# Performance work log

Measured on AMD Instinct MI355X. Metric: run time of the kernel, lower is better.

Reference implementation:

```python
import jax, jax.numpy as jnp
import numpy as np

N_NODES = 50000
N_EDGES = 600000
IN_DIM, HID, OUT_DIM = 128, 128, 64
LN_EPS = 1e-5


def setup_inputs() -> dict:
    key = jax.random.key(0)
    ks = jax.random.split(key, 10)
    def glorot(k, shape):
        lim = np.sqrt(6.0 / (shape[0] + shape[1]))
        return jax.random.uniform(k, shape, jnp.float32, -lim, lim)
    return {
        "x": jax.random.normal(ks[0], (N_NODES, IN_DIM), jnp.float32),
        "src": jax.random.randint(ks[1], (N_EDGES,), 0, N_NODES, jnp.int32),
        "dst": jax.random.randint(ks[2], (N_EDGES,), 0, N_NODES, jnp.int32),
        "W0": glorot(ks[3], (IN_DIM, HID)), "b0": jnp.zeros((HID,), jnp.float32),
        "W1": glorot(ks[4], (HID, HID)),    "b1": jnp.zeros((HID,), jnp.float32),
        "W2": glorot(ks[5], (HID, OUT_DIM)),"b2": jnp.zeros((OUT_DIM,), jnp.float32),
        "ln_scale": jnp.ones((HID,), jnp.float32),
        "ln_bias": jnp.zeros((HID,), jnp.float32),
    }


def _degree_norms(src, dst):
    ones = jnp.ones((src.shape[0],), jnp.float32)
    deg_out = jax.ops.segment_sum(ones, src, num_segments=N_NODES)
    deg_in = jax.ops.segment_sum(ones, dst, num_segments=N_NODES)
    # DGL clamps degree to min 1 for norm='both'
    out_norm = jnp.clip(deg_out, 1.0, None) ** -0.5
    in_norm = jnp.clip(deg_in, 1.0, None) ** -0.5
    return out_norm, in_norm


def _graph_conv(h, src, dst, out_norm, in_norm, W, b):
    # norm='both': scale src side, SpMM aggregate, scale dst side, then affine
    h = h * out_norm[:, None]
    h = h @ W  # apply weight first (mathematically identical, smaller messages when out<in)
    agg = jax.ops.segment_sum(h[src], dst, num_segments=N_NODES)  # [N, D]
    return agg * in_norm[:, None] + b


def _layernorm(h, scale, bias):
    mu = jnp.mean(h, axis=-1, keepdims=True)
    var = jnp.var(h, axis=-1, keepdims=True)
    return (h - mu) * jax.lax.rsqrt(var + LN_EPS) * scale + bias


def reference(x, src, dst, W0, b0, W1, b1, W2, b2, ln_scale, ln_bias):
    out_norm, in_norm = _degree_norms(src, dst)
    # dropout is identity in eval mode
    h = jax.nn.relu(_graph_conv(x, src, dst, out_norm, in_norm, W0, b0))
    h = _layernorm(h, ln_scale, ln_bias)
    h = jax.nn.relu(_graph_conv(h, src, dst, out_norm, in_norm, W1, b1))
    h = _layernorm(h, ln_scale, ln_bias)
    # last layer: encoding=True -> keep activation; no norm after last layer
    h = jax.nn.relu(_graph_conv(h, src, dst, out_norm, in_norm, W2, b2))
    return h
```

## Files before the change

kernel.cpp:

```cpp
#include <hip/hip_runtime.h>
#include <hip/hip_fp16.h>

#define NN 50000
#define NE 600000
#define LN_EPS 1e-5f
#define SCAN_B 49
#define RANGES 8
#define RSZ 6250
#define CHUNKS 16
#define CSZ 37500

typedef __attribute__((ext_vector_type(8))) _Float16 half8;
typedef __attribute__((ext_vector_type(4))) float floatx4;

__device__ __align__(16) __half g_h0[NN * 128];
__device__ __align__(16) __half g_h1[NN * 128];
__device__ __align__(16) int g_deg_in[NN];
__device__ float g_out_norm[NN];
__device__ float g_in_norm[NN];
__device__ int g_rowptr[NN + 1];
__device__ int g_esrc[NE];
__device__ int g_blocksum[SCAN_B];
__device__ int g_blockoff[SCAN_B];
__device__ int g_pout[CHUNKS * NN];
__device__ int g_pin[CHUNKS * NN];
__device__ int g_base[CHUNKS * NN];

__device__ __forceinline__ __half* hbuf(int i) { return i ? g_h1 : g_h0; }

__global__ __launch_bounds__(256) void histo_kernel(const int* __restrict__ src,
                                                    const int* __restrict__ dst) {
    __shared__ int h_out[RSZ];
    __shared__ int h_in[RSZ];
    int c = blockIdx.x / RANGES, r = blockIdx.x % RANGES;
    int lo = r * RSZ;
    for (int i = threadIdx.x; i < RSZ; i += 256) { h_out[i] = 0; h_in[i] = 0; }
    __syncthreads();
    const int4* s4 = (const int4*)(src + c * CSZ);
    const int4* d4 = (const int4*)(dst + c * CSZ);
    for (int i = threadIdx.x; i < CSZ / 4; i += 256) {
        int4 s = s4[i], d = d4[i];
        int v;
        v = s.x - lo; if ((unsigned)v < RSZ) atomicAdd(&h_out[v], 1);
        v = s.y - lo; if ((unsigned)v < RSZ) atomicAdd(&h_out[v], 1);
        v = s.z - lo; if ((unsigned)v < RSZ) atomicAdd(&h_out[v], 1);
        v = s.w - lo; if ((unsigned)v < RSZ) atomicAdd(&h_out[v], 1);
        v = d.x - lo; if ((unsigned)v < RSZ) atomicAdd(&h_in[v], 1);
        v = d.y - lo; if ((unsigned)v < RSZ) atomicAdd(&h_in[v], 1);
        v = d.z - lo; if ((unsigned)v < RSZ) atomicAdd(&h_in[v], 1);
        v = d.w - lo; if ((unsigned)v < RSZ) atomicAdd(&h_in[v], 1);
    }
    __syncthreads();
    for (int i = threadIdx.x; i < RSZ; i += 256) {
        g_pout[c * NN + lo + i] = h_out[i];
        g_pin[c * NN + lo + i]  = h_in[i];
    }
}

__global__ __launch_bounds__(256) void sums_norms_kernel() {
    int n = blockIdx.x * 256 + threadIdx.x;
    if (n >= NN) return;
    int so = 0, si = 0;
#pragma unroll
    for (int c = 0; c < CHUNKS; ++c) { so += g_pout[c * NN + n]; si += g_pin[c * NN + n]; }
    g_deg_in[n] = si;
    g_out_norm[n] = rsqrtf((float)max(so, 1));
    g_in_norm[n]  = rsqrtf((float)max(si, 1));
}

__global__ __launch_bounds__(256) void scan_phase1() {
    __shared__ int wsum[4];
    int b = blockIdx.x, t = threadIdx.x;
    int base = b * 1024 + t * 4;
    int s = 0;
    if (base + 3 < NN) {
        int4 v = *(const int4*)&g_deg_in[base];
        s = v.x + v.y + v.z + v.w;
    } else {
#pragma unroll
        for (int k = 0; k < 4; ++k)
            if (base + k < NN) s += g_deg_in[base + k];
    }
#pragma unroll
    for (int off = 32; off; off >>= 1) s += __shfl_xor(s, off, 64);
    if ((t & 63) == 0) wsum[t >> 6] = s;
    __syncthreads();
    if (t == 0) g_blocksum[b] = wsum[0] + wsum[1] + wsum[2] + wsum[3];
}

__global__ __launch_bounds__(64) void scan_phase2() {
    int lane = threadIdx.x;
    int own = (lane < SCAN_B) ? g_blocksum[lane] : 0;
    int v = own;
#pragma unroll
    for (int off = 1; off < 64; off <<= 1) {
        int n = __shfl_up(v, off, 64);
        if (lane >= off) v += n;
    }
    if (lane < SCAN_B) g_blockoff[lane] = v - own;
    if (lane == SCAN_B - 1) g_rowptr[NN] = v;
}

__global__ __launch_bounds__(256) void scan_phase3() {
    __shared__ int sums[256];
    int b = blockIdx.x, t = threadIdx.x;
    int base = b * 1024 + t * 4;
    int v[4];
#pragma unroll
    for (int k = 0; k < 4; ++k) v[k] = (base + k < NN) ? g_deg_in[base + k] : 0;
    int tsum = v[0] + v[1] + v[2] + v[3];
    sums[t] = tsum;
    __syncthreads();
    for (int off = 1; off < 256; off <<= 1) {
        int add = (t >= off) ? sums[t - off] : 0;
        __syncthreads();
        sums[t] += add;
        __syncthreads();
    }
    int excl = sums[t] - tsum + g_blockoff[b];
#pragma unroll
    for (int k = 0; k < 4; ++k) {
        int idx = base + k;
        if (idx < NN) g_rowptr[idx] = excl;
        excl += v[k];
    }
}

__global__ __launch_bounds__(256) void base_kernel() {
    int n = blockIdx.x * 256 + threadIdx.x;
    if (n >= NN) return;
    int run = g_rowptr[n];
#pragma unroll
    for (int c = 0; c < CHUNKS; ++c) {
        g_base[c * NN + n] = run;
        run += g_pin[c * NN + n];
    }
}

__global__ __launch_bounds__(256) void place_lds_kernel(const int* __restrict__ src,
                                                        const int* __restrict__ dst) {
    __shared__ int cur[RSZ];
    int c = blockIdx.x / RANGES, r = blockIdx.x % RANGES;
    int lo = r * RSZ;
    for (int i = threadIdx.x; i < RSZ; i += 256) cur[i] = g_base[c * NN + lo + i];
    __syncthreads();
    const int4* s4 = (const int4*)(src + c * CSZ);
    const int4* d4 = (const int4*)(dst + c * CSZ);
    for (int i = threadIdx.x; i < CSZ / 4; i += 256) {
        int4 s = s4[i], d = d4[i];
        int v, p;
        v = d.x - lo; if ((unsigned)v < RSZ) { p = atomicAdd(&cur[v], 1); g_esrc[p] = s.x; }
        v = d.y - lo; if ((unsigned)v < RSZ) { p = atomicAdd(&cur[v], 1); g_esrc[p] = s.y; }
        v = d.z - lo; if ((unsigned)v < RSZ) { p = atomicAdd(&cur[v], 1); g_esrc[p] = s.z; }
        v = d.w - lo; if ((unsigned)v < RSZ) { p = atomicAdd(&cur[v], 1); g_esrc[p] = s.w; }
    }
}

template <int N, bool AEXT>
__global__ __launch_bounds__(256) void gemm_mfma(const float* __restrict__ Aext,
                                                 int a_ib, int c_ib,
                                                 const float* __restrict__ Wg,
                                                 int M) {
    constexpr int NT = N / 16;
    constexpr int LOGN = (N == 128) ? 7 : 6;
    __shared__ _Float16 Wl[128 * N];

    const int tid = threadIdx.x;
    for (int e = tid; e < 128 * N; e += 256) {
        int k = e >> LOGN, n = e & (N - 1);
        Wl[(((k >> 3) * N + n) << 3) + (k & 7)] = (_Float16)Wg[e];
    }
    __syncthreads();

    const int wv = tid >> 6, lane = tid & 63;
    const int quad = lane >> 4, mrow = lane & 15;
    const int rowbase = blockIdx.x * 64 + wv * 16;
    const int arow0 = rowbase + mrow;
    const int arow = (arow0 < M) ? arow0 : (M - 1);

    floatx4 acc[NT] = {};
    const __half* Ah = AEXT ? nullptr : hbuf(a_ib);

#pragma unroll
    for (int kk = 0; kk < 4; ++kk) {
        const int k0 = kk * 32 + quad * 8;
        half8 afrag;
        if (AEXT) {
            const float4* ap = (const float4*)(Aext + (size_t)arow * 128 + k0);
            float4 f0 = ap[0], f1 = ap[1];
            afrag[0] = (_Float16)f0.x; afrag[1] = (_Float16)f0.y;
            afrag[2] = (_Float16)f0.z; afrag[3] = (_Float16)f0.w;
            afrag[4] = (_Float16)f1.x; afrag[5] = (_Float16)f1.y;
            afrag[6] = (_Float16)f1.z; afrag[7] = (_Float16)f1.w;
        } else {
            afrag = *(const half8*)(Ah + (size_t)arow * 128 + k0);
        }
#pragma unroll
        for (int nt = 0; nt < NT; ++nt) {
            half8 bfrag = *(const half8*)&Wl[(((kk * 4 + quad) * N + nt * 16 + mrow) << 3)];
            acc[nt] = __builtin_amdgcn_mfma_f32_16x16x32_f16(afrag, bfrag, acc[nt], 0, 0, 0);
        }
    }

    __half* C = hbuf(c_ib);
#pragma unroll
    for (int r = 0; r < 4; ++r) {
        int crow = rowbase + quad * 4 + r;
        if (crow < M) {
            float s = g_out_norm[crow];
#pragma unroll
            for (int nt = 0; nt < NT; ++nt) {
                float v = acc[nt][r] * s;
                C[(size_t)crow * N + nt * 16 + mrow] = __float2half_rn(v);
            }
        }
    }
}

__global__ __launch_bounds__(256) void gather_ln_kernel(int s_ib, int d_ib,
                                                        const float* __restrict__ b,
                                                        const float* __restrict__ ln_s,
                                                        const float* __restrict__ ln_b) {
    int wave = threadIdx.x >> 6;
    int lane = threadIdx.x & 63;
    int node = blockIdx.x * 4 + wave;
    if (node >= NN) return;
    const unsigned int* Hu = (const unsigned int*)hbuf(s_ib);
    int beg = g_rowptr[node], end = g_rowptr[node + 1];
    float ax = 0.f, ay = 0.f;
    int j = beg;
    for (; j + 3 < end; j += 4) {
        int s0 = g_esrc[j], s1 = g_esrc[j + 1], s2 = g_esrc[j + 2], s3 = g_esrc[j + 3];
        unsigned int u0 = Hu[s0 * 64 + lane];
        unsigned int u1 = Hu[s1 * 64 + lane];
        unsigned int u2 = Hu[s2 * 64 + lane];
        unsigned int u3 = Hu[s3 * 64 + lane];
        float2 f0 = __half22float2(*(const __half2*)&u0);
        float2 f1 = __half22float2(*(const __half2*)&u1);
        float2 f2 = __half22float2(*(const __half2*)&u2);
        float2 f3 = __half22float2(*(const __half2*)&u3);
        ax += (f0.x + f1.x) + (f2.x + f3.x);
        ay += (f0.y + f1.y) + (f2.y + f3.y);
    }
    for (; j < end; ++j) {
        unsigned int u = Hu[g_esrc[j] * 64 + lane];
        float2 f = __half22float2(*(const __half2*)&u);
        ax += f.x; ay += f.y;
    }
    float nrm = g_in_norm[node];
    int c = lane * 2;
    float vx = fmaxf(ax * nrm + b[c], 0.f);
    float vy = fmaxf(ay * nrm + b[c + 1], 0.f);
    float s = vx + vy;
    float sq = vx * vx + vy * vy;
#pragma unroll
    for (int off = 32; off > 0; off >>= 1) {
        s  += __shfl_xor(s, off, 64);
        sq += __shfl_xor(sq, off, 64);
    }
    float mean = s * (1.f / 128.f);
    float var = sq * (1.f / 128.f) - mean * mean;
    float inv = rsqrtf(var + LN_EPS);
    float ox = (vx - mean) * inv * ln_s[c] + ln_b[c];
    float oy = (vy - mean) * inv * ln_s[c + 1] + ln_b[c + 1];
    __half2 h = __floats2half2_rn(ox, oy);
    ((unsigned int*)hbuf(d_ib))[node * 64 + lane] = *(const unsigned int*)&h;
}

__global__ __launch_bounds__(256) void GCN_63831803953156_kernel(int s_ib,
                                                                 const float* __restrict__ b2,
                                                                 float* __restrict__ out) {
    int wave = threadIdx.x >> 6;
    int lane = threadIdx.x & 63;
    int node = blockIdx.x * 4 + wave;
    if (node >= NN) return;
    const unsigned short* Hs = (const unsigned short*)hbuf(s_ib);
    int beg = g_rowptr[node], end = g_rowptr[node + 1];
    float acc = 0.f;
    int j = beg;
    for (; j + 3 < end; j += 4) {
        int s0 = g_esrc[j], s1 = g_esrc[j + 1], s2 = g_esrc[j + 2], s3 = g_esrc[j + 3];
        unsigned short u0 = Hs[s0 * 64 + lane];
        unsigned short u1 = Hs[s1 * 64 + lane];
        unsigned short u2 = Hs[s2 * 64 + lane];
        unsigned short u3 = Hs[s3 * 64 + lane];
        acc += (__half2float(*(const __half*)&u0) + __half2float(*(const __half*)&u1)) +
               (__half2float(*(const __half*)&u2) + __half2float(*(const __half*)&u3));
    }
    for (; j < end; ++j) {
        unsigned short u = Hs[g_esrc[j] * 64 + lane];
        acc += __half2float(*(const __half*)&u);
    }
    float v = fmaxf(acc * g_in_norm[node] + b2[lane], 0.f);
    out[node * 64 + lane] = v;
}

extern "C" void kernel_launch(void* const* d_in, const int* in_sizes, int n_in,
                              void* d_out, int out_size, void* d_ws, size_t ws_size,
                              hipStream_t stream) {
    const float* x   = (const float*)d_in[0];
    const int* src   = (const int*)d_in[1];
    const int* dst   = (const int*)d_in[2];
    const float* W0  = (const float*)d_in[3];
    const float* b0  = (const float*)d_in[4];
    const float* W1  = (const float*)d_in[5];
    const float* b1  = (const float*)d_in[6];
    const float* W2  = (const float*)d_in[7];
    const float* b2  = (const float*)d_in[8];
    const float* ln_s = (const float*)d_in[9];
    const float* ln_b = (const float*)d_in[10];
    (void)d_ws; (void)ws_size; (void)in_sizes; (void)n_in; (void)out_size;

    histo_kernel<<<CHUNKS * RANGES, 256, 0, stream>>>(src, dst);
    sums_norms_kernel<<<(NN + 255) / 256, 256, 0, stream>>>();
    scan_phase1<<<SCAN_B, 256, 0, stream>>>();
    scan_phase2<<<1, 64, 0, stream>>>();
    scan_phase3<<<SCAN_B, 256, 0, stream>>>();
    base_kernel<<<(NN + 255) / 256, 256, 0, stream>>>();
    place_lds_kernel<<<CHUNKS * RANGES, 256, 0, stream>>>(src, dst);

    const int GB = (NN + 63) / 64;

    gemm_mfma<128, true><<<GB, 256, 0, stream>>>(x, -1, 0, W0, NN);
    gather_ln_kernel<<<(NN + 3) / 4, 256, 0, stream>>>(0, 1, b0, ln_s, ln_b);

    gemm_mfma<128, false><<<GB, 256, 0, stream>>>(nullptr, 1, 0, W1, NN);
    gather_ln_kernel<<<(NN + 3) / 4, 256, 0, stream>>>(0, 1, b1, ln_s, ln_b);

    gemm_mfma<64, false><<<GB, 256, 0, stream>>>(nullptr, 1, 0, W2, NN);
    GCN_63831803953156_kernel<<<(NN + 3) / 4, 256, 0, stream>>>(0, b2, (float*)d_out);
}
```

Baseline: 286.0 us.

## Gather multiple nodes per wave with wider loads and fuse CSR-build kernels

The gather kernels now split each 64-lane wave into sub-groups that each process a separate node, reading 8-byte vectors per lane instead of 2- or 4-byte values. This doubles or quadruples the number of independent rows in flight per wave and widens the memory transactions. The degree-sum, norm and scan-phase1 kernels are merged into one 1024-thread kernel, and the base-offset computation is folded into scan phase 3, which removes two launches. The node bounds checks are dropped, so correctness relies on NN being divisible by 8 and 16.

```diff
diff --git a/kernel.cpp b/kernel.cpp
--- a/kernel.cpp
+++ b/kernel.cpp
@@ -57,35 +57,30 @@
     }
 }
 
-__global__ __launch_bounds__(256) void sums_norms_kernel() {
-    int n = blockIdx.x * 256 + threadIdx.x;
-    if (n >= NN) return;
-    int so = 0, si = 0;
-#pragma unroll
-    for (int c = 0; c < CHUNKS; ++c) { so += g_pout[c * NN + n]; si += g_pin[c * NN + n]; }
-    g_deg_in[n] = si;
-    g_out_norm[n] = rsqrtf((float)max(so, 1));
-    g_in_norm[n]  = rsqrtf((float)max(si, 1));
-}
-
-__global__ __launch_bounds__(256) void scan_phase1() {
-    __shared__ int wsum[4];
+__global__ __launch_bounds__(1024) void deg_scan1_kernel() {
+    __shared__ int wsum[16];
     int b = blockIdx.x, t = threadIdx.x;
-    int base = b * 1024 + t * 4;
-    int s = 0;
-    if (base + 3 < NN) {
-        int4 v = *(const int4*)&g_deg_in[base];
-        s = v.x + v.y + v.z + v.w;
-    } else {
-#pragma unroll
-        for (int k = 0; k < 4; ++k)
-            if (base + k < NN) s += g_deg_in[base + k];
-    }
+    int n = b * 1024 + t;
+    int si = 0;
+    if (n < NN) {
+        int so = 0;
+#pragma unroll
+        for (int c = 0; c < CHUNKS; ++c) { so += g_pout[c * NN + n]; si += g_pin[c * NN + n]; }
+        g_deg_in[n] = si;
+        g_out_norm[n] = rsqrtf((float)max(so, 1));
+        g_in_norm[n]  = rsqrtf((float)max(si, 1));
+    }
+    int s = si;
 #pragma unroll
     for (int off = 32; off; off >>= 1) s += __shfl_xor(s, off, 64);
     if ((t & 63) == 0) wsum[t >> 6] = s;
     __syncthreads();
-    if (t == 0) g_blocksum[b] = wsum[0] + wsum[1] + wsum[2] + wsum[3];
+    if (t < 16) {
+        int v = wsum[t];
+#pragma unroll
+        for (int off = 8; off; off >>= 1) v += __shfl_xor(v, off, 16);
+        if (t == 0) g_blocksum[b] = v;
+    }
 }
 
 __global__ __launch_bounds__(64) void scan_phase2() {
@@ -101,7 +96,7 @@
     if (lane == SCAN_B - 1) g_rowptr[NN] = v;
 }
 
-__global__ __launch_bounds__(256) void scan_phase3() {
+__global__ __launch_bounds__(256) void scan3_base_kernel() {
     __shared__ int sums[256];
     int b = blockIdx.x, t = threadIdx.x;
     int base = b * 1024 + t * 4;
@@ -121,19 +116,16 @@
 #pragma unroll
     for (int k = 0; k < 4; ++k) {
         int idx = base + k;
-        if (idx < NN) g_rowptr[idx] = excl;
+        if (idx < NN) {
+            g_rowptr[idx] = excl;
+            int run = excl;
+#pragma unroll
+            for (int c = 0; c < CHUNKS; ++c) {
+                g_base[c * NN + idx] = run;
+                run += g_pin[c * NN + idx];
+            }
+        }
         excl += v[k];
-    }
-}
-
-__global__ __launch_bounds__(256) void base_kernel() {
-    int n = blockIdx.x * 256 + threadIdx.x;
-    if (n >= NN) return;
-    int run = g_rowptr[n];
-#pragma unroll
-    for (int c = 0; c < CHUNKS; ++c) {
-        g_base[c * NN + n] = run;
-        run += g_pin[c * NN + n];
     }
 }
 
@@ -223,48 +215,58 @@
                                                         const float* __restrict__ ln_b) {
     int wave = threadIdx.x >> 6;
     int lane = threadIdx.x & 63;
-    int node = blockIdx.x * 4 + wave;
-    if (node >= NN) return;
-    const unsigned int* Hu = (const unsigned int*)hbuf(s_ib);
+    int sub = lane >> 5, sl = lane & 31;
+    int node = blockIdx.x * 8 + wave * 2 + sub;
+    const uint2* Hu = (const uint2*)hbuf(s_ib);
     int beg = g_rowptr[node], end = g_rowptr[node + 1];
-    float ax = 0.f, ay = 0.f;
+    float a0 = 0.f, a1 = 0.f, a2 = 0.f, a3 = 0.f;
     int j = beg;
     for (; j + 3 < end; j += 4) {
         int s0 = g_esrc[j], s1 = g_esrc[j + 1], s2 = g_esrc[j + 2], s3 = g_esrc[j + 3];
-        unsigned int u0 = Hu[s0 * 64 + lane];
-        unsigned int u1 = Hu[s1 * 64 + lane];
-        unsigned int u2 = Hu[s2 * 64 + lane];
-        unsigned int u3 = Hu[s3 * 64 + lane];
-        float2 f0 = __half22float2(*(const __half2*)&u0);
-        float2 f1 = __half22float2(*(const __half2*)&u1);
-        float2 f2 = __half22float2(*(const __half2*)&u2);
-        float2 f3 = __half22float2(*(const __half2*)&u3);
-        ax += (f0.x + f1.x) + (f2.x + f3.x);
-        ay += (f0.y + f1.y) + (f2.y + f3.y);
+        uint2 u0 = Hu[s0 * 32 + sl];
+        uint2 u1 = Hu[s1 * 32 + sl];
+        uint2 u2 = Hu[s2 * 32 + sl];
+        uint2 u3 = Hu[s3 * 32 + sl];
+        float2 p0 = __half22float2(*(const __half2*)&u0.x), q0 = __half22float2(*(const __half2*)&u0.y);
+        float2 p1 = __half22float2(*(const __half2*)&u1.x), q1 = __half22float2(*(const __half2*)&u1.y);
+        float2 p2 = __half22float2(*(const __half2*)&u2.x), q2 = __half22float2(*(const __half2*)&u2.y);
+        float2 p3 = __half22float2(*(const __half2*)&u3.x), q3 = __half22float2(*(const __half2*)&u3.y);
+        a0 += (p0.x + p1.x) + (p2.x + p3.x);
+        a1 += (p0.y + p1.y) + (p2.y + p3.y);
+        a2 += (q0.x + q1.x) + (q2.x + q3.x);
+        a3 += (q0.y + q1.y) + (q2.y + q3.y);
     }
     for (; j < end; ++j) {
-        unsigned int u = Hu[g_esrc[j] * 64 + lane];
-        float2 f = __half22float2(*(const __half2*)&u);
-        ax += f.x; ay += f.y;
+        uint2 u = Hu[g_esrc[j] * 32 + sl];
+        float2 p = __half22float2(*(const __half2*)&u.x), q = __half22float2(*(const __half2*)&u.y);
+        a0 += p.x; a1 += p.y; a2 += q.x; a3 += q.y;
     }
     float nrm = g_in_norm[node];
-    int c = lane * 2;
-    float vx = fmaxf(ax * nrm + b[c], 0.f);
-    float vy = fmaxf(ay * nrm + b[c + 1], 0.f);
-    float s = vx + vy;
-    float sq = vx * vx + vy * vy;
-#pragma unroll
-    for (int off = 32; off > 0; off >>= 1) {
+    float4 bb = ((const float4*)b)[sl];
+    float v0 = fmaxf(a0 * nrm + bb.x, 0.f);
+    float v1 = fmaxf(a1 * nrm + bb.y, 0.f);
+    float v2 = fmaxf(a2 * nrm + bb.z, 0.f);
+    float v3 = fmaxf(a3 * nrm + bb.w, 0.f);
+    float s = (v0 + v1) + (v2 + v3);
+    float sq = (v0 * v0 + v1 * v1) + (v2 * v2 + v3 * v3);
+#pragma unroll
+    for (int off = 16; off > 0; off >>= 1) {
         s  += __shfl_xor(s, off, 64);
         sq += __shfl_xor(sq, off, 64);
     }
     float mean = s * (1.f / 128.f);
     float var = sq * (1.f / 128.f) - mean * mean;
     float inv = rsqrtf(var + LN_EPS);
-    float ox = (vx - mean) * inv * ln_s[c] + ln_b[c];
-    float oy = (vy - mean) * inv * ln_s[c + 1] + ln_b[c + 1];
-    __half2 h = __floats2half2_rn(ox, oy);
-    ((unsigned int*)hbuf(d_ib))[node * 64 + lane] = *(const unsigned int*)&h;
+    float4 ls = ((const float4*)ln_s)[sl];
+    float4 lb = ((const float4*)ln_b)[sl];
+    float o0 = (v0 - mean) * inv * ls.x + lb.x;
+    float o1 = (v1 - mean) * inv * ls.y + lb.y;
+    float o2 = (v2 - mean) * inv * ls.z + lb.z;
+    float o3 = (v3 - mean) * inv * ls.w + lb.w;
+    __half2 h0 = __floats2half2_rn(o0, o1);
+    __half2 h1 = __floats2half2_rn(o2, o3);
+    uint2 o = make_uint2(*(const unsigned int*)&h0, *(const unsigned int*)&h1);
+    ((uint2*)hbuf(d_ib))[node * 32 + sl] = o;
 }
 
 __global__ __launch_bounds__(256) void GCN_63831803953156_kernel(int s_ib,
@@ -272,27 +274,40 @@
                                                                  float* __restrict__ out) {
     int wave = threadIdx.x >> 6;
     int lane = threadIdx.x & 63;
-    int node = blockIdx.x * 4 + wave;
-    if (node >= NN) return;
-    const unsigned short* Hs = (const unsigned short*)hbuf(s_ib);
+    int sub = lane >> 4, sl = lane & 15;
+    int node = blockIdx.x * 16 + wave * 4 + sub;
+    const uint2* Hu = (const uint2*)hbuf(s_ib);
     int beg = g_rowptr[node], end = g_rowptr[node + 1];
-    float acc = 0.f;
+    float a0 = 0.f, a1 = 0.f, a2 = 0.f, a3 = 0.f;
     int j = beg;
     for (; j + 3 < end; j += 4) {
         int s0 = g_esrc[j], s1 = g_esrc[j + 1], s2 = g_esrc[j + 2], s3 = g_esrc[j + 3];
-        unsigned short u0 = Hs[s0 * 64 + lane];
-        unsigned short u1 = Hs[s1 * 64 + lane];
-        unsigned short u2 = Hs[s2 * 64 + lane];
-        unsigned short u3 = Hs[s3 * 64 + lane];
-        acc += (__half2float(*(const __half*)&u0) + __half2float(*(const __half*)&u1)) +
-               (__half2float(*(const __half*)&u2) + __half2float(*(const __half*)&u3));
+        uint2 u0 = Hu[s0 * 16 + sl];
+        uint2 u1 = Hu[s1 * 16 + sl];
+        uint2 u2 = Hu[s2 * 16 + sl];
+        uint2 u3 = Hu[s3 * 16 + sl];
+        float2 p0 = __half22float2(*(const __half2*)&u0.x), q0 = __half22float2(*(const __half2*)&u0.y);
+        float2 p1 = __half22float2(*(const __half2*)&u1.x), q1 = __half22float2(*(const __half2*)&u1.y);
+        float2 p2 = __half22float2(*(const __half2*)&u2.x), q2 = __half22float2(*(const __half2*)&u2.y);
+        float2 p3 = __half22float2(*(const __half2*)&u3.x), q3 = __half22float2(*(const __half2*)&u3.y);
+        a0 += (p0.x + p1.x) + (p2.x + p3.x);
+        a1 += (p0.y + p1.y) + (p2.y + p3.y);
+        a2 += (q0.x + q1.x) + (q2.x + q3.x);
+        a3 += (q0.y + q1.y) + (q2.y + q3.y);
     }
     for (; j < end; ++j) {
-        unsigned short u = Hs[g_esrc[j] * 64 + lane];
-        acc += __half2float(*(const __half*)&u);
-    }
-    float v = fmaxf(acc * g_in_norm[node] + b2[lane], 0.f);
-    out[node * 64 + lane] = v;
+        uint2 u = Hu[g_esrc[j] * 16 + sl];
+        float2 p = __half22float2(*(const __half2*)&u.x), q = __half22float2(*(const __half2*)&u.y);
+        a0 += p.x; a1 += p.y; a2 += q.x; a3 += q.y;
+    }
+    float nrm = g_in_norm[node];
+    float4 bb = ((const float4*)b2)[sl];
+    float4 o;
+    o.x = fmaxf(a0 * nrm + bb.x, 0.f);
+    o.y = fmaxf(a1 * nrm + bb.y, 0.f);
+    o.z = fmaxf(a2 * nrm + bb.z, 0.f);
+    o.w = fmaxf(a3 * nrm + bb.w, 0.f);
+    ((float4*)out)[node * 16 + sl] = o;
 }
 
 extern "C" void kernel_launch(void* const* d_in, const int* in_sizes, int n_in,
@@ -312,21 +327,19 @@
     (void)d_ws; (void)ws_size; (void)in_sizes; (void)n_in; (void)out_size;
 
     histo_kernel<<<CHUNKS * RANGES, 256, 0, stream>>>(src, dst);
-    sums_norms_kernel<<<(NN + 255) / 256, 256, 0, stream>>>();
-    scan_phase1<<<SCAN_B, 256, 0, stream>>>();
+    deg_scan1_kernel<<<SCAN_B, 1024, 0, stream>>>();
     scan_phase2<<<1, 64, 0, stream>>>();
-    scan_phase3<<<SCAN_B, 256, 0, stream>>>();
-    base_kernel<<<(NN + 255) / 256, 256, 0, stream>>>();
+    scan3_base_kernel<<<SCAN_B, 256, 0, stream>>>();
     place_lds_kernel<<<CHUNKS * RANGES, 256, 0, stream>>>(src, dst);
 
     const int GB = (NN + 63) / 64;
 
     gemm_mfma<128, true><<<GB, 256, 0, stream>>>(x, -1, 0, W0, NN);
-    gather_ln_kernel<<<(NN + 3) / 4, 256, 0, stream>>>(0, 1, b0, ln_s, ln_b);
+    gather_ln_kernel<<<NN / 8, 256, 0, stream>>>(0, 1, b0, ln_s, ln_b);
 
     gemm_mfma<128, false><<<GB, 256, 0, stream>>>(nullptr, 1, 0, W1, NN);
-    gather_ln_kernel<<<(NN + 3) / 4, 256, 0, stream>>>(0, 1, b1, ln_s, ln_b);
+    gather_ln_kernel<<<NN / 8, 256, 0, stream>>>(0, 1, b1, ln_s, ln_b);
 
     gemm_mfma<64, false><<<GB, 256, 0, stream>>>(nullptr, 1, 0, W2, NN);
-    GCN_63831803953156_kernel<<<(NN + 3) / 4, 256, 0, stream>>>(0, b2, (float*)d_out);
-}
+    GCN_63831803953156_kernel<<<NN / 16, 256, 0, stream>>>(0, b2, (float*)d_out);
+}
```

Result: faster. 267.2 us (-6.6%).
